# Performance work log

Measured on AMD Instinct MI355X. Metric: run time of the kernel, lower is better.

Reference implementation:

```python
import jax, jax.numpy as jnp
import numpy as np

SOFTMAX_T = 1.0  # softmax_temperature


def setup_inputs() -> dict:
    key = jax.random.key(0)
    k1, k2, k3 = jax.random.split(key, 3)
    B, D, N = 2048, 64, 100000
    state = jax.random.normal(k1, (B, D), dtype=jnp.float32)
    item_embeddings = jax.random.normal(k2, (N, D), dtype=jnp.float32)
    item_index = jax.random.randint(k3, (B, 1), 0, N, dtype=jnp.int64)
    return {"state": state, "item_index": item_index, "item_embeddings": item_embeddings}


def reference(state, item_index, item_embeddings):
    # logits[b, n] = sum_d state[b, d] * E[n, d] / T  -> one batched matmul
    logits = jnp.einsum("bd,nd->bn", state, item_embeddings) / SOFTMAX_T
    log_items_prob = jax.nn.log_softmax(logits, axis=1)  # [B, N]
    # gather selected item log-probs per batch row -> [B, 1]
    log_item_prob = jnp.take_along_axis(log_items_prob, item_index, axis=1)
    return log_item_prob
```

## Files before the change

### kernel.cpp

```cpp
#include <hip/hip_runtime.h>
#include <math.h>


typedef short short8 __attribute__((ext_vector_type(8)));
typedef float f32x4 __attribute__((ext_vector_type(4)));

constexpr int kD = 64;
constexpr int kChunks = 128;
constexpr int kChunkItems = 784;
constexpr float kLog2e = 1.44269504088896340736f;

static __device__ inline unsigned short bf16_rne(float x) {
    unsigned int u = __builtin_bit_cast(unsigned int, x);
    u = (u + 0x7FFFu + ((u >> 16) & 1u)) >> 16;
    return (unsigned short)u;
}
static __device__ inline float bf16_f32(unsigned short h) {
    unsigned int u = ((unsigned int)h) << 16;
    return __builtin_bit_cast(float, u);
}

__global__ __launch_bounds__(256) void prep_e_kernel(
    const float* __restrict__ src, unsigned short* __restrict__ hi,
    unsigned short* __restrict__ lo, int total4, float scale)
{
    int i = blockIdx.x * 256 + threadIdx.x;
    if (i >= total4) return;
    float4 v = ((const float4*)src)[i];
    v.x *= scale; v.y *= scale; v.z *= scale; v.w *= scale;
    ushort4 h, l;
    h.x = bf16_rne(v.x); l.x = bf16_rne(v.x - bf16_f32(h.x));
    h.y = bf16_rne(v.y); l.y = bf16_rne(v.y - bf16_f32(h.y));
    h.z = bf16_rne(v.z); l.z = bf16_rne(v.z - bf16_f32(h.z));
    h.w = bf16_rne(v.w); l.w = bf16_rne(v.w - bf16_f32(h.w));
    ((ushort4*)hi)[i] = h;
    ((ushort4*)lo)[i] = l;
}

#define MFMA16(a, b, c) __builtin_amdgcn_mfma_f32_16x16x32_bf16((a), (b), (c), 0, 0, 0)

__global__ __launch_bounds__(256) void lse_mfma_kernel(
    const unsigned short* __restrict__ Sh,
    const unsigned short* __restrict__ Sl,
    const unsigned short* __restrict__ Eh,
    const unsigned short* __restrict__ El,
    float* __restrict__ part,
    int N, int Btot)
{
    const int wave = threadIdx.x >> 6;
    const int lane = threadIdx.x & 63;
    const int l15  = lane & 15;
    const int lhi  = lane >> 4;
    const int chunk = blockIdx.x;
    const int rowg  = blockIdx.y;
    const int r0 = rowg * 256 + wave * 64;

    const int n0 = chunk * kChunkItems;
    const int cnt = min(kChunkItems, N - n0);
    const int ntiles = cnt >> 4;

    short8 A[4][2][2];
    #pragma unroll
    for (int rt = 0; rt < 4; ++rt) {
        const int row = r0 + rt * 16 + l15;
        const size_t base = (size_t)row * kD + lhi * 8;
        A[rt][0][0] = *(const short8*)(Sh + base);
        A[rt][0][1] = *(const short8*)(Sh + base + 32);
        A[rt][1][0] = *(const short8*)(Sl + base);
        A[rt][1][1] = *(const short8*)(Sl + base + 32);
    }

    float acc[4][4];
    #pragma unroll
    for (int rt = 0; rt < 4; ++rt)
        #pragma unroll
        for (int j = 0; j < 4; ++j) acc[rt][j] = 0.f;

    const int voff = l15 * kD + lhi * 8;
    const unsigned short* eh = Eh + (size_t)n0 * kD + voff;
    const unsigned short* el = El + (size_t)n0 * kD + voff;

    for (int t = 0; t < ntiles; ++t) {
        const size_t o = (size_t)t * 1024;
        short8 Bh0 = *(const short8*)(eh + o);
        short8 Bh1 = *(const short8*)(eh + o + 32);
        short8 Bl0 = *(const short8*)(el + o);
        short8 Bl1 = *(const short8*)(el + o + 32);

        const f32x4 z = {0.f, 0.f, 0.f, 0.f};
        f32x4 ca[4], cb[4];
        #pragma unroll
        for (int rt = 0; rt < 4; ++rt) ca[rt] = MFMA16(A[rt][0][0], Bh0, z);
        #pragma unroll
        for (int rt = 0; rt < 4; ++rt) cb[rt] = MFMA16(A[rt][1][0], Bh0, z);
        #pragma unroll
        for (int rt = 0; rt < 4; ++rt) ca[rt] = MFMA16(A[rt][0][1], Bh1, ca[rt]);
        #pragma unroll
        for (int rt = 0; rt < 4; ++rt) cb[rt] = MFMA16(A[rt][1][1], Bh1, cb[rt]);
        #pragma unroll
        for (int rt = 0; rt < 4; ++rt) ca[rt] = MFMA16(A[rt][0][0], Bl0, ca[rt]);
        #pragma unroll
        for (int rt = 0; rt < 4; ++rt) ca[rt] = MFMA16(A[rt][0][1], Bl1, ca[rt]);

        #pragma unroll
        for (int rt = 0; rt < 4; ++rt)
            #pragma unroll
            for (int j = 0; j < 4; ++j)
                acc[rt][j] += __builtin_amdgcn_exp2f(ca[rt][j] + cb[rt][j]);
    }

    #pragma unroll
    for (int rt = 0; rt < 4; ++rt) {
        #pragma unroll
        for (int j = 0; j < 4; ++j) {
            float v = acc[rt][j];
            v += __shfl_xor(v, 1, 64);
            v += __shfl_xor(v, 2, 64);
            v += __shfl_xor(v, 4, 64);
            v += __shfl_xor(v, 8, 64);
            if (l15 == 0) {
                const int row = r0 + rt * 16 + lhi * 4 + j;
                part[(size_t)chunk * Btot + row] = v;
            }
        }
    }
}

__global__ __launch_bounds__(256) void finalize_kernel(
    const float* __restrict__ state,
    const float* __restrict__ emb,
    const int* __restrict__ idx,
    const float* __restrict__ part,
    float* __restrict__ out, int Btot)
{
    const int wave = threadIdx.x >> 6;
    const int lane = threadIdx.x & 63;
    const int row  = blockIdx.x * 4 + wave;

    const float* pr = part + row;
    float sv = pr[(size_t)lane * Btot] + pr[(size_t)(lane + 64) * Btot];
    #pragma unroll
    for (int o = 32; o; o >>= 1) sv += __shfl_xor(sv, o, 64);
    float lse = logf(sv);

    int id = idx[row];
    float d = state[(size_t)row * kD + lane] * emb[(size_t)id * kD + lane];
    #pragma unroll
    for (int o = 32; o; o >>= 1) d += __shfl_xor(d, o, 64);

    if (lane == 0) out[row] = d - lse;
}

extern "C" void kernel_launch(void* const* d_in, const int* in_sizes, int n_in,
                              void* d_out, int out_size, void* d_ws, size_t ws_size,
                              hipStream_t stream) {
    const float* state = (const float*)d_in[0];
    const int*   idx   = (const int*)d_in[1];
    const float* emb   = (const float*)d_in[2];
    float*       out   = (float*)d_out;

    const int B = in_sizes[0] / kD;
    const int N = in_sizes[2] / kD;

    char* ws = (char*)d_ws;
    size_t szE = (size_t)N * kD * sizeof(unsigned short);
    size_t szS = (size_t)B * kD * sizeof(unsigned short);
    unsigned short* Eh = (unsigned short*)ws;                  ws += szE;
    unsigned short* El = (unsigned short*)ws;                  ws += szE;
    unsigned short* Sh = (unsigned short*)ws;                  ws += szS;
    unsigned short* Sl = (unsigned short*)ws;                  ws += szS;
    float* part = (float*)ws;

    int e4 = N * kD / 4;
    prep_e_kernel<<<(e4 + 255) / 256, 256, 0, stream>>>(emb, Eh, El, e4, 1.0f);
    int s4 = B * kD / 4;
    prep_e_kernel<<<(s4 + 255) / 256, 256, 0, stream>>>(state, Sh, Sl, s4, kLog2e);

    dim3 grid(kChunks, B / 256);
    lse_mfma_kernel<<<grid, 256, 0, stream>>>(Sh, Sl, Eh, El, part, N, B);

    finalize_kernel<<<B / 4, 256, 0, stream>>>(state, emb, idx, part, out, B);
}
```

Measured before the change: 205.4 us.

## Stage embedding tiles through LDS with async double buffering and XCD-aware mapping

Reorders the bf16 hi/lo embedding split into a tiled, XOR-swizzled interleaved layout. The LSE kernel now streams those tiles into shared memory with global_load_lds, double buffered across stages, instead of each wave loading directly from global memory. Blocks are remapped so that chunks sharing embedding data are grouped per XCD, which should improve L2 reuse across the eight row groups. The code hardcodes N=100000 (125 chunks of 50 tiles) and the grid size, so it only handles this exact shape, and it adds a block-wide barrier every stage.

Measured after the change: 179.0 us. 1.15x faster.

```diff
diff --git a/kernel.cpp b/kernel.cpp
--- a/kernel.cpp
+++ b/kernel.cpp
@@ -6,8 +6,10 @@
 typedef float f32x4 __attribute__((ext_vector_type(4)));
 
 constexpr int kD = 64;
-constexpr int kChunks = 128;
-constexpr int kChunkItems = 784;
+constexpr int kChunks = 125;
+constexpr int kTilesPerChunk = 50;
+constexpr int kST = 5;
+constexpr int kStages = 10;
 constexpr float kLog2e = 1.44269504088896340736f;
 
 static __device__ inline unsigned short bf16_rne(float x) {
@@ -20,7 +22,7 @@
     return __builtin_bit_cast(float, u);
 }
 
-__global__ __launch_bounds__(256) void prep_e_kernel(
+__global__ __launch_bounds__(256) void prep_s_kernel(
     const float* __restrict__ src, unsigned short* __restrict__ hi,
     unsigned short* __restrict__ lo, int total4, float scale)
 {
@@ -37,27 +39,50 @@
     ((ushort4*)lo)[i] = l;
 }
 
+__global__ __launch_bounds__(256) void prep_e_kernel(
+    const float* __restrict__ src, unsigned short* __restrict__ EhEl, int N)
+{
+    int i = blockIdx.x * 256 + threadIdx.x;
+    if (i >= N * 16) return;
+    int n  = i >> 4;
+    int dq = i & 15;
+    float4 v = *(const float4*)(src + (size_t)n * kD + dq * 4);
+    ushort4 h, l;
+    h.x = bf16_rne(v.x); l.x = bf16_rne(v.x - bf16_f32(h.x));
+    h.y = bf16_rne(v.y); l.y = bf16_rne(v.y - bf16_f32(h.y));
+    h.z = bf16_rne(v.z); l.z = bf16_rne(v.z - bf16_f32(h.z));
+    h.w = bf16_rne(v.w); l.w = bf16_rne(v.w - bf16_f32(h.w));
+    int tile = n >> 4, item = n & 15;
+    unsigned hb = ((unsigned)(item * 128 + dq * 8)) ^ ((unsigned)(item & 7) << 4);
+    char* base = (char*)EhEl + (size_t)tile * 4096;
+    *(ushort4*)(base + hb)        = h;
+    *(ushort4*)(base + 2048 + hb) = l;
+}
+
 #define MFMA16(a, b, c) __builtin_amdgcn_mfma_f32_16x16x32_bf16((a), (b), (c), 0, 0, 0)
 
 __global__ __launch_bounds__(256) void lse_mfma_kernel(
     const unsigned short* __restrict__ Sh,
     const unsigned short* __restrict__ Sl,
-    const unsigned short* __restrict__ Eh,
-    const unsigned short* __restrict__ El,
+    const unsigned short* __restrict__ EhEl,
     float* __restrict__ part,
-    int N, int Btot)
-{
-    const int wave = threadIdx.x >> 6;
-    const int lane = threadIdx.x & 63;
+    int Btot)
+{
+    __shared__ unsigned short lds[2][kST * 2048];
+
+    const int tid  = threadIdx.x;
+    const int wave = tid >> 6;
+    const int lane = tid & 63;
     const int l15  = lane & 15;
     const int lhi  = lane >> 4;
-    const int chunk = blockIdx.x;
-    const int rowg  = blockIdx.y;
+
+    const int bid  = blockIdx.x;
+    const int xcd  = bid & 7;
+    const int rowg = (bid >> 3) & 7;
+    const int chunk = (bid >> 6) * 8 + xcd;
+    if (chunk >= kChunks) return;
+
     const int r0 = rowg * 256 + wave * 64;
-
-    const int n0 = chunk * kChunkItems;
-    const int cnt = min(kChunkItems, N - n0);
-    const int ntiles = cnt >> 4;
 
     short8 A[4][2][2];
     #pragma unroll
@@ -76,38 +101,62 @@
         #pragma unroll
         for (int j = 0; j < 4; ++j) acc[rt][j] = 0.f;
 
-    const int voff = l15 * kD + lhi * 8;
-    const unsigned short* eh = Eh + (size_t)n0 * kD + voff;
-    const unsigned short* el = El + (size_t)n0 * kD + voff;
-
-    for (int t = 0; t < ntiles; ++t) {
-        const size_t o = (size_t)t * 1024;
-        short8 Bh0 = *(const short8*)(eh + o);
-        short8 Bh1 = *(const short8*)(eh + o + 32);
-        short8 Bl0 = *(const short8*)(el + o);
-        short8 Bl1 = *(const short8*)(el + o + 32);
-
-        const f32x4 z = {0.f, 0.f, 0.f, 0.f};
-        f32x4 ca[4], cb[4];
+    const unsigned xorv = (unsigned)((l15 & 7) << 4);
+    const int o_h0 = (int)(((unsigned)(l15 * 128 + lhi * 16))      ^ xorv);
+    const int o_h1 = (int)(((unsigned)(l15 * 128 + lhi * 16 + 64)) ^ xorv);
+
+    const unsigned short* src = EhEl + (size_t)chunk * kTilesPerChunk * 2048;
+
+#define STAGE(buf, s) { \
+    const unsigned short* sp_ = src + (size_t)(s) * (kST * 2048); \
+    _Pragma("unroll") \
+    for (int c = 0; c < kST; ++c) { \
+        __builtin_amdgcn_global_load_lds( \
+            (const __attribute__((address_space(1))) void*)(sp_ + (size_t)(c * 256 + tid) * 8), \
+            (__attribute__((address_space(3))) void*)&lds[buf][(c * 256 + wave * 64) * 8], \
+            16, 0, 0); \
+    } }
+
+    STAGE(0, 0);
+    __syncthreads();
+
+    for (int s = 0; s < kStages; ++s) {
+        const int cur = s & 1;
+        if (s + 1 < kStages) STAGE(cur ^ 1, s + 1);
+
+        const char* lb = (const char*)lds[cur];
         #pragma unroll
-        for (int rt = 0; rt < 4; ++rt) ca[rt] = MFMA16(A[rt][0][0], Bh0, z);
-        #pragma unroll
-        for (int rt = 0; rt < 4; ++rt) cb[rt] = MFMA16(A[rt][1][0], Bh0, z);
-        #pragma unroll
-        for (int rt = 0; rt < 4; ++rt) ca[rt] = MFMA16(A[rt][0][1], Bh1, ca[rt]);
-        #pragma unroll
-        for (int rt = 0; rt < 4; ++rt) cb[rt] = MFMA16(A[rt][1][1], Bh1, cb[rt]);
-        #pragma unroll
-        for (int rt = 0; rt < 4; ++rt) ca[rt] = MFMA16(A[rt][0][0], Bl0, ca[rt]);
-        #pragma unroll
-        for (int rt = 0; rt < 4; ++rt) ca[rt] = MFMA16(A[rt][0][1], Bl1, ca[rt]);
-
-        #pragma unroll
-        for (int rt = 0; rt < 4; ++rt)
-            #pragma unroll
-            for (int j = 0; j < 4; ++j)
-                acc[rt][j] += __builtin_amdgcn_exp2f(ca[rt][j] + cb[rt][j]);
+        for (int tt = 0; tt < kST; ++tt) {
+            const char* tp = lb + tt * 4096;
+            short8 Bh0 = *(const short8*)(tp + o_h0);
+            short8 Bh1 = *(const short8*)(tp + o_h1);
+            short8 Bl0 = *(const short8*)(tp + 2048 + o_h0);
+            short8 Bl1 = *(const short8*)(tp + 2048 + o_h1);
+
+            const f32x4 z = {0.f, 0.f, 0.f, 0.f};
+            f32x4 ca[4], cb[4];
+            #pragma unroll
+            for (int rt = 0; rt < 4; ++rt) ca[rt] = MFMA16(A[rt][0][0], Bh0, z);
+            #pragma unroll
+            for (int rt = 0; rt < 4; ++rt) cb[rt] = MFMA16(A[rt][1][0], Bh0, z);
+            #pragma unroll
+            for (int rt = 0; rt < 4; ++rt) ca[rt] = MFMA16(A[rt][0][1], Bh1, ca[rt]);
+            #pragma unroll
+            for (int rt = 0; rt < 4; ++rt) cb[rt] = MFMA16(A[rt][1][1], Bh1, cb[rt]);
+            #pragma unroll
+            for (int rt = 0; rt < 4; ++rt) ca[rt] = MFMA16(A[rt][0][0], Bl0, ca[rt]);
+            #pragma unroll
+            for (int rt = 0; rt < 4; ++rt) ca[rt] = MFMA16(A[rt][0][1], Bl1, ca[rt]);
+
+            #pragma unroll
+            for (int rt = 0; rt < 4; ++rt)
+                #pragma unroll
+                for (int j = 0; j < 4; ++j)
+                    acc[rt][j] += __builtin_amdgcn_exp2f(ca[rt][j] + cb[rt][j]);
+        }
+        __syncthreads();
     }
+#undef STAGE
 
     #pragma unroll
     for (int rt = 0; rt < 4; ++rt) {
@@ -138,7 +187,9 @@
     const int row  = blockIdx.x * 4 + wave;
 
     const float* pr = part + row;
-    float sv = pr[(size_t)lane * Btot] + pr[(size_t)(lane + 64) * Btot];
+    float sv = 0.f;
+    if (lane < kChunks)      sv += pr[(size_t)lane * Btot];
+    if (lane + 64 < kChunks) sv += pr[(size_t)(lane + 64) * Btot];
     #pragma unroll
     for (int o = 32; o; o >>= 1) sv += __shfl_xor(sv, o, 64);
     float lse = logf(sv);
@@ -163,21 +214,18 @@
     const int N = in_sizes[2] / kD;
 
     char* ws = (char*)d_ws;
-    size_t szE = (size_t)N * kD * sizeof(unsigned short);
+    size_t szE = (size_t)N * kD * 2 * sizeof(unsigned short);
     size_t szS = (size_t)B * kD * sizeof(unsigned short);
-    unsigned short* Eh = (unsigned short*)ws;                  ws += szE;
-    unsigned short* El = (unsigned short*)ws;                  ws += szE;
-    unsigned short* Sh = (unsigned short*)ws;                  ws += szS;
-    unsigned short* Sl = (unsigned short*)ws;                  ws += szS;
+    unsigned short* EhEl = (unsigned short*)ws;                ws += szE;
+    unsigned short* Sh   = (unsigned short*)ws;                ws += szS;
+    unsigned short* Sl   = (unsigned short*)ws;                ws += szS;
     float* part = (float*)ws;
 
-    int e4 = N * kD / 4;
-    prep_e_kernel<<<(e4 + 255) / 256, 256, 0, stream>>>(emb, Eh, El, e4, 1.0f);
+    prep_e_kernel<<<(N * 16 + 255) / 256, 256, 0, stream>>>(emb, EhEl, N);
     int s4 = B * kD / 4;
-    prep_e_kernel<<<(s4 + 255) / 256, 256, 0, stream>>>(state, Sh, Sl, s4, kLog2e);
-
-    dim3 grid(kChunks, B / 256);
-    lse_mfma_kernel<<<grid, 256, 0, stream>>>(Sh, Sl, Eh, El, part, N, B);
+    prep_s_kernel<<<(s4 + 255) / 256, 256, 0, stream>>>(state, Sh, Sl, s4, kLog2e);
+
+    lse_mfma_kernel<<<1024, 256, 0, stream>>>(Sh, Sl, EhEl, part, B);
 
     finalize_kernel<<<B / 4, 256, 0, stream>>>(state, emb, idx, part, out, B);
 }
```
